# Performance work log

Measured on AMD Instinct MI355X. Metric: run time of the kernel, lower is better.

## Reference

```python
import jax, jax.numpy as jnp
import numpy as np
import math

B, S, HID = 1, 2048, 2048
H, KVH, HD = 16, 4, 128
LEVEL = 256


def _rope_tables(seq_len, dim, dtype=jnp.float32):
    inv_freq = 1.0 / (10000.0 ** (np.arange(0, dim, 2, dtype=np.float32) / dim))
    ang = np.arange(seq_len, dtype=np.float32)[:, None] * inv_freq[None, :]  # [S, HD/2]
    emb = np.concatenate([ang, ang], axis=-1)  # [S, HD]
    return jnp.asarray(np.cos(emb), dtype)[None], jnp.asarray(np.sin(emb), dtype)[None]


def setup_inputs() -> dict:
    key = jax.random.key(0)
    ks = jax.random.split(key, 6)
    hidden_states = jax.random.normal(ks[0], (B, S, HID), jnp.float32)
    w_std = 1.0 / math.sqrt(HID)
    Wq = jax.random.normal(ks[1], (H * HD, HID), jnp.float32) * w_std
    Wk = jax.random.normal(ks[2], (KVH * HD, HID), jnp.float32) * w_std
    Wv = jax.random.normal(ks[3], (KVH * HD, HID), jnp.float32) * w_std
    Wo = jax.random.normal(ks[4], (HID, H * HD), jnp.float32) * w_std
    cos, sin = _rope_tables(S, HD)
    # additive causal mask [1,1,S,S]
    tri = jnp.tril(jnp.ones((S, S), jnp.bool_))
    attention_mask = jnp.where(tri, 0.0, -1e9).astype(jnp.float32)[None, None]
    return {
        "hidden_states": hidden_states,
        "Wq": Wq, "Wk": Wk, "Wv": Wv, "Wo": Wo,
        "s_q": jnp.full((1,), 0.05, jnp.float32),
        "s_k": jnp.full((1,), 0.05, jnp.float32),
        "s_v": jnp.full((1,), 0.05, jnp.float32),
        "s_attn": jnp.full((1,), 0.004, jnp.float32),
        "s_out": jnp.full((1,), 0.02, jnp.float32),
        "cos": cos, "sin": sin,
        "attention_mask": attention_mask,
    }


def _lsq(x, s, level, sym):
    # LSQ fake-quant: learned per-tensor step s, STE round, LSQ grad-scale on s.
    if sym:
        qn, qp = -level // 2, level // 2 - 1
    else:
        qn, qp = 0, level - 1
    g = 1.0 / math.sqrt(x.size * qp)          # LSQ gradient scale (static)
    s = jnp.abs(s)
    s_eff = s * g + jax.lax.stop_gradient(s - s * g)  # fwd = s, bwd grad *= g
    v = jnp.clip(x / s_eff, qn, qp)
    q = v + jax.lax.stop_gradient(jnp.round(v) - v)   # STE round
    return q * s_eff


def _rotate_half(x):
    x1, x2 = jnp.split(x, 2, axis=-1)
    return jnp.concatenate([-x2, x1], axis=-1)


def _attn_fwd(hidden_states, Wq, Wk, Wv, Wo, s_q, s_k, s_v, s_attn, s_out,
              cos, sin, attention_mask):
    b, s_len, _ = hidden_states.shape
    # projections -> [B, heads, S, HD]
    q = (hidden_states @ Wq.T).reshape(b, s_len, H, HD).transpose(0, 2, 1, 3)
    q = _lsq(q, s_q, LEVEL, sym=True)
    k = (hidden_states @ Wk.T).reshape(b, s_len, KVH, HD).transpose(0, 2, 1, 3)
    k = _lsq(k, s_k, LEVEL, sym=True)
    v = (hidden_states @ Wv.T).reshape(b, s_len, KVH, HD).transpose(0, 2, 1, 3)
    v = _lsq(v, s_v, LEVEL, sym=True)
    # RoPE (after quant, matching source order)
    c, si = cos[:, None], sin[:, None]  # [B,1,S,HD]
    q = q * c + _rotate_half(q) * si
    k = k * c + _rotate_half(k) * si
    # GQA repeat
    groups = H // KVH
    k = jnp.repeat(k, groups, axis=1)
    v = jnp.repeat(v, groups, axis=1)
    scores = jnp.einsum("bhqd,bhkd->bhqk", q, k) / math.sqrt(HD)
    scores = scores + attention_mask[:, :, :, :s_len]
    attn = jax.nn.softmax(scores.astype(jnp.float32), axis=-1).astype(q.dtype)
    attn = _lsq(attn, s_attn, LEVEL, sym=False)
    out = jnp.einsum("bhqk,bhkd->bhqd", attn, v)
    out = _lsq(out, s_out, LEVEL, sym=False)
    out = out.transpose(0, 2, 1, 3).reshape(b, s_len, H * HD)
    out = out @ Wo.T
    return out, attn


def reference(hidden_states, Wq, Wk, Wv, Wo, s_q, s_k, s_v, s_attn, s_out,
              cos, sin, attention_mask):
    return _attn_fwd(hidden_states, Wq, Wk, Wv, Wo, s_q, s_k, s_v, s_attn,
                     s_out, cos, sin, attention_mask)
```

## Files before the change

kernel.cpp:

```cpp
#include <hip/hip_runtime.h>
#include <math.h>

#define S_LEN 2048
#define HID_DIM 2048
#define NH 16
#define NKVH 4
#define HD 128
#define QD (NH*HD)
#define KD (NKVH*HD)
#define NQKV 3072

typedef _Float16 half8_t __attribute__((ext_vector_type(8)));
typedef _Float16 half4_t __attribute__((ext_vector_type(4)));
typedef float f32x4 __attribute__((ext_vector_type(4)));

#define BM 128
#define BN 128
#define BK 32
#define KCHUNK 512

typedef const __attribute__((address_space(1))) char gas_char;
typedef __attribute__((address_space(3))) char las_char;
#define GL16(gp, lp) __builtin_amdgcn_global_load_lds((gas_char*)(gp), (las_char*)(lp), 16, 0, 0)

template<int LA, int LB, bool AF32, bool PSM, bool ATOMK>
__global__ __launch_bounds__(256)
void gemm_f16(const void* __restrict__ Ap, const _Float16* __restrict__ Alo,
              int lda, long long strA,
              const _Float16* __restrict__ Bhi, const _Float16* __restrict__ Blo,
              int ldb, long long strB, int divB,
              void* __restrict__ Cp, int ldc, long long strC,
              int K, float scale_c, const float* sc1, const float* sc2,
              const float* preAp,
              int qmode, const float* q1, const float* q2, const float* q3,
              int causal, int triK, float* __restrict__ pml)
{
    int bz = blockIdx.z;
    int m0 = blockIdx.y * BM;
    int n0 = ATOMK ? 0 : blockIdx.x * BN;
    if (causal && n0 > m0 + (BM - 1)) return;
    int Keff = K;
    if (triK && (m0 + BM) < Keff) Keff = m0 + BM;

    int kbeg = 0, kend = Keff;
    if constexpr (ATOMK) {
        kbeg = blockIdx.x * KCHUNK;
        kend = min(Keff, kbeg + KCHUNK);
        if (kbeg >= kend) return;
    }

    const _Float16* Ahi = AF32 ? nullptr : (const _Float16*)Ap + bz * strA;
    const _Float16* AloP = (LA == 2) ? Alo + bz * strA : nullptr;
    const float* Af = AF32 ? (const float*)Ap + bz * strA : nullptr;
    const _Float16* BhiP = Bhi + (long long)(bz / divB) * strB;
    const _Float16* BloP = (LB == 2) ? Blo + (long long)(bz / divB) * strB : nullptr;
    float* Cf = (float*)Cp + bz * strC;
    _Float16* Ch = (_Float16*)Cp + bz * strC;

    float preA = 1.f;
    if (AF32) preA = 1.f / fabsf(preAp[0]);

    __shared__ _Float16 lds[(LA + LB) * 4096];
    _Float16* As0 = lds;
    _Float16* As1 = lds + 4096;
    _Float16* Bs0 = lds + LA * 4096;
    _Float16* Bs1 = lds + (LA + 1) * 4096;

    int t = threadIdx.x;
    int srow = t >> 2;
    int gsw = (srow >> 1) & 3;
    int gc = ((t & 3) ^ gsw) * 8;
    int w = t >> 6, lane = t & 63;
    int wm = (w >> 1) * 64, wn = (w & 1) * 64;
    int lr = lane & 15, lg = lane >> 4;
    int fco = ((lg ^ ((lr >> 1) & 3))) * 8;

    f32x4 acc[4][4];
    #pragma unroll
    for (int i = 0; i < 4; ++i)
        #pragma unroll
        for (int j = 0; j < 4; ++j)
            acc[i][j] = (f32x4){0.f, 0.f, 0.f, 0.f};

    for (int k0 = kbeg; k0 < kend; k0 += BK) {
        f32x4 aF[2][2];
        if constexpr (AF32) {
            #pragma unroll
            for (int rep = 0; rep < 2; ++rep) {
                long long ai = (long long)(m0 + rep * 64 + srow) * lda + k0 + gc;
                aF[rep][0] = *(const f32x4*)&Af[ai];
                aF[rep][1] = *(const f32x4*)&Af[ai + 4];
            }
        }
        __syncthreads();
        #pragma unroll
        for (int rep = 0; rep < 2; ++rep) {
            int row = rep * 64 + srow;
            int lo = rep * 2048 + t * 8;
            if constexpr (!AF32) {
                long long ai = (long long)(m0 + row) * lda + k0 + gc;
                GL16(Ahi + ai, As0 + lo);
                if constexpr (LA == 2) GL16(AloP + ai, As1 + lo);
            }
            long long bi = (long long)(n0 + row) * ldb + k0 + gc;
            GL16(BhiP + bi, Bs0 + lo);
            if constexpr (LB == 2) GL16(BloP + bi, Bs1 + lo);
        }
        if constexpr (AF32) {
            #pragma unroll
            for (int rep = 0; rep < 2; ++rep) {
                half8_t h;
                #pragma unroll
                for (int e = 0; e < 4; ++e) {
                    h[e]     = (_Float16)(aF[rep][0][e] * preA);
                    h[e + 4] = (_Float16)(aF[rep][1][e] * preA);
                }
                *(half8_t*)&As0[rep * 2048 + t * 8] = h;
            }
        }
        __syncthreads();

        half8_t a0[4], b0[4];
        #pragma unroll
        for (int i = 0; i < 4; ++i) a0[i] = *(const half8_t*)&As0[(wm + i*16 + lr) * 32 + fco];
        #pragma unroll
        for (int j = 0; j < 4; ++j) b0[j] = *(const half8_t*)&Bs0[(wn + j*16 + lr) * 32 + fco];
        #pragma unroll
        for (int i = 0; i < 4; ++i)
            #pragma unroll
            for (int j = 0; j < 4; ++j)
                acc[i][j] = __builtin_amdgcn_mfma_f32_16x16x32_f16(a0[i], b0[j], acc[i][j], 0, 0, 0);
        if constexpr (LB == 2) {
            half8_t b1[4];
            #pragma unroll
            for (int j = 0; j < 4; ++j) b1[j] = *(const half8_t*)&Bs1[(wn + j*16 + lr) * 32 + fco];
            #pragma unroll
            for (int i = 0; i < 4; ++i)
                #pragma unroll
                for (int j = 0; j < 4; ++j)
                    acc[i][j] = __builtin_amdgcn_mfma_f32_16x16x32_f16(a0[i], b1[j], acc[i][j], 0, 0, 0);
        }
        if constexpr (LA == 2) {
            half8_t a1[4];
            #pragma unroll
            for (int i = 0; i < 4; ++i) a1[i] = *(const half8_t*)&As1[(wm + i*16 + lr) * 32 + fco];
            #pragma unroll
            for (int i = 0; i < 4; ++i)
                #pragma unroll
                for (int j = 0; j < 4; ++j)
                    acc[i][j] = __builtin_amdgcn_mfma_f32_16x16x32_f16(a1[i], b0[j], acc[i][j], 0, 0, 0);
        }
    }

    if constexpr (ATOMK) {
        #pragma unroll
        for (int i = 0; i < 4; ++i)
            #pragma unroll
            for (int j = 0; j < 4; ++j)
                #pragma unroll
                for (int r = 0; r < 4; ++r) {
                    long long row = m0 + wm + i * 16 + lg * 4 + r;
                    long long col = n0 + wn + j * 16 + lr;
                    atomicAdd(&Cf[row * (long long)ldc + col], acc[i][j][r]);
                }
        return;
    }

    float se = scale_c;
    if (sc1) se *= fabsf(sc1[0]);
    if (sc2) se *= fabsf(sc2[0]);
    float sv = 1.f;
    if (qmode == 3) {
        const float* sp = (n0 < 2048) ? q1 : ((n0 < 2560) ? q2 : q3);
        sv = fabsf(sp[0]);
        qmode = 1;
    } else if (qmode) {
        sv = fabsf(q1[0]);
    }

    #pragma unroll
    for (int i = 0; i < 4; ++i)
        #pragma unroll
        for (int j = 0; j < 4; ++j)
            #pragma unroll
            for (int r = 0; r < 4; ++r) {
                long long row = m0 + wm + i * 16 + lg * 4 + r;
                long long col = n0 + wn + j * 16 + lr;
                float v = acc[i][j][r] * se;
                if (qmode == 0) {
                    Cf[row * (long long)ldc + col] = v;
                } else if (qmode == 1) {
                    float u = rintf(fminf(fmaxf(v / sv, -128.f), 127.f));
                    Ch[row * (long long)ldc + col] = (_Float16)u;
                } else {
                    float u = rintf(fminf(fmaxf(v / sv, 0.f), 255.f));
                    Ch[row * (long long)ldc + col] = (_Float16)u;
                }
            }

    if constexpr (PSM) {
        int cb64 = (n0 + wn) >> 6;
        #pragma unroll
        for (int i = 0; i < 4; ++i)
            #pragma unroll
            for (int r = 0; r < 4; ++r) {
                int row = m0 + wm + i * 16 + lg * 4 + r;
                float vv[4];
                float mloc = -INFINITY;
                #pragma unroll
                for (int j = 0; j < 4; ++j) {
                    int col = n0 + wn + j * 16 + lr;
                    float v = acc[i][j][r] * se;
                    vv[j] = (col <= row) ? v : -INFINITY;
                    mloc = fmaxf(mloc, vv[j]);
                }
                #pragma unroll
                for (int o = 1; o < 16; o <<= 1) mloc = fmaxf(mloc, __shfl_xor(mloc, o));
                float sloc = 0.f;
                #pragma unroll
                for (int j = 0; j < 4; ++j) sloc += expf(vv[j] - mloc);
                #pragma unroll
                for (int o = 1; o < 16; o <<= 1) sloc += __shfl_xor(sloc, o);
                if (lr == 0) {
                    long long idx = (((long long)bz * S_LEN + row) * 32 + cb64) * 2;
                    pml[idx] = mloc;
                    pml[idx + 1] = sloc;
                }
            }
    }
}

__global__ __launch_bounds__(256)
void reduce_ml(const float* __restrict__ pml, float* __restrict__ fml)
{
    int id = blockIdx.x * 256 + threadIdx.x;
    int r = id & (S_LEN - 1);
    int nb = (r >> 6) + 1;
    float m = -INFINITY, l = 0.f;
    const float* p = pml + (long long)id * 64;
    for (int cb = 0; cb < nb; ++cb) {
        float mp = p[cb * 2], lp = p[cb * 2 + 1];
        float mn = fmaxf(m, mp);
        l = l * expf(m - mn) + lp * expf(mp - mn);
        m = mn;
    }
    fml[id * 2] = m;
    fml[id * 2 + 1] = l;
}

__global__ __launch_bounds__(256)
void finalize_quant(float* __restrict__ attn, const float* __restrict__ fml,
                    const float* __restrict__ s_at_p)
{
    int row = blockIdx.x;
    int q = row & (S_LEN - 1);
    float* p = attn + (long long)row * S_LEN;
    float m = fml[row * 2];
    float l = fml[row * 2 + 1];
    float sa = fabsf(s_at_p[0]);
    int t = threadIdx.x;
    #pragma unroll
    for (int c = t * 4; c < S_LEN; c += 1024) {
        f32x4 v = *(const f32x4*)&p[c];
        f32x4 o;
        #pragma unroll
        for (int e = 0; e < 4; ++e) {
            float u = 0.f;
            if (c + e <= q) {
                float pr = expf(v[e] - m) / l;
                u = rintf(fminf(fmaxf(pr / sa, 0.f), 255.f));
            }
            o[e] = u * sa;
        }
        *(f32x4*)&p[c] = o;
    }
}

__global__ __launch_bounds__(256)
void quant_ao(const float* __restrict__ acc, _Float16* __restrict__ ao,
              const float* sa_p, const float* sv_p, const float* so_p)
{
    int i = blockIdx.x * 256 + threadIdx.x;
    float seo = fabsf(sa_p[0]) * fabsf(sv_p[0]) / fabsf(so_p[0]);
    f32x4 v = ((const f32x4*)acc)[i];
    half4_t o;
    #pragma unroll
    for (int e = 0; e < 4; ++e)
        o[e] = (_Float16)rintf(fminf(fmaxf(v[e] * seo, 0.f), 255.f));
    ((half4_t*)ao)[i] = o;
}

__global__ void split_f16(const float* __restrict__ in, _Float16* __restrict__ hi,
                          _Float16* __restrict__ lo, int n4)
{
    int i = blockIdx.x * 256 + threadIdx.x;
    if (i >= n4) return;
    f32x4 v = ((const f32x4*)in)[i];
    half4_t h, l;
    #pragma unroll
    for (int e = 0; e < 4; ++e) {
        h[e] = (_Float16)v[e];
        l[e] = (_Float16)(v[e] - (float)h[e]);
    }
    ((half4_t*)hi)[i] = h;
    ((half4_t*)lo)[i] = l;
}

__global__ void rope_f16(const _Float16* __restrict__ codes, int ldc_, int colOff,
                         const float* __restrict__ cosT,
                         const float* __restrict__ sinT,
                         _Float16* __restrict__ ohi, _Float16* __restrict__ olo, int nh)
{
    long long idx = (long long)blockIdx.x * 256 + threadIdx.x;
    int d = idx & (HD - 1);
    long long tt = idx >> 7;
    int h = (int)(tt % nh);
    int s = (int)(tt / nh);
    long long base = (long long)s * ldc_ + colOff + h * HD;
    float x = (float)codes[base + d];
    float other = (d < 64) ? -(float)codes[base + d + 64] : (float)codes[base + d - 64];
    float o = x * cosT[s * HD + d] + other * sinT[s * HD + d];
    _Float16 hf = (_Float16)o;
    long long oi = ((long long)h * S_LEN + s) * HD + d;
    ohi[oi] = hf;
    olo[oi] = (_Float16)(o - (float)hf);
}

__global__ __launch_bounds__(256)
void transpose_vf16(const _Float16* __restrict__ in, _Float16* __restrict__ outp)
{
    __shared__ _Float16 tile[64][72];
    int s0 = blockIdx.x * 64, d0 = blockIdx.y * 64, h = blockIdx.z;
    int t = threadIdx.x;
    int rr = t >> 4, cc = (t & 15) * 4;
    #pragma unroll
    for (int r = 0; r < 4; ++r) {
        half4_t v = *(const half4_t*)&in[(long long)(s0 + rr + 16*r) * NQKV + 2560 + h * HD + d0 + cc];
        *(half4_t*)&tile[rr + 16*r][cc] = v;
    }
    __syncthreads();
    #pragma unroll
    for (int r = 0; r < 4; ++r) {
        int dr = rr + 16 * r;
        half4_t o = { tile[cc+0][dr], tile[cc+1][dr], tile[cc+2][dr], tile[cc+3][dr] };
        *(half4_t*)&outp[((long long)h * HD + d0 + dr) * S_LEN + s0 + cc] = o;
    }
}

extern "C" void kernel_launch(void* const* d_in, const int* in_sizes, int n_in,
                              void* d_out, int out_size, void* d_ws, size_t ws_size,
                              hipStream_t stream)
{
    const float* hs    = (const float*)d_in[0];
    const float* Wq    = (const float*)d_in[1];
    const float* Wk    = (const float*)d_in[2];
    const float* Wv    = (const float*)d_in[3];
    const float* Wo    = (const float*)d_in[4];
    const float* s_q   = (const float*)d_in[5];
    const float* s_k   = (const float*)d_in[6];
    const float* s_v   = (const float*)d_in[7];
    const float* s_at  = (const float*)d_in[8];
    const float* s_out = (const float*)d_in[9];
    const float* cosT  = (const float*)d_in[10];
    const float* sinT  = (const float*)d_in[11];

    float* out  = (float*)d_out;
    float* attn = out + (long long)S_LEN * HID_DIM;

    const long long M1 = 1LL * 1024 * 1024;
    const long long M4 = 4LL * M1;
    const long long M6 = 6LL * M1;

    _Float16* wsh   = (_Float16*)d_ws;
    _Float16* qr_hi = wsh;
    _Float16* qr_lo = qr_hi + M4;
    _Float16* kr_hi = qr_lo + M4;
    _Float16* kr_lo = kr_hi + M1;
    _Float16* vT    = kr_lo + M1;
    _Float16* ao    = vT + M1;
    _Float16* Wo_hi = ao + M4;
    _Float16* Wo_lo = Wo_hi + M4;
    float*    ao_acc = (float*)(Wo_lo + M4);

    _Float16* sc      = (_Float16*)attn;
    _Float16* hs_hi   = sc;
    _Float16* hs_lo   = hs_hi + M4;
    _Float16* Whi     = hs_lo + M4;
    _Float16* Wlo     = Whi + M6;
    _Float16* qkvcode = Wlo + M6;

    float* pml = out;
    float* fml = out + 2LL * 1024 * 1024;

    dim3 blk(256);
    const float iscale = 0.08838834764831845f;

    split_f16<<<4096, blk, 0, stream>>>(hs, hs_hi, hs_lo, 1024*1024);
    split_f16<<<4096, blk, 0, stream>>>(Wq, Whi, Wlo, 1024*1024);
    split_f16<<<1024, blk, 0, stream>>>(Wk, Whi + 2048LL*2048, Wlo + 2048LL*2048, 256*1024);
    split_f16<<<1024, blk, 0, stream>>>(Wv, Whi + 2560LL*2048, Wlo + 2560LL*2048, 256*1024);
    split_f16<<<4096, blk, 0, stream>>>(Wo, Wo_hi, Wo_lo, 1024*1024);

    gemm_f16<2,2,false,false,false><<<dim3(NQKV/BN, S_LEN/BM, 1), blk, 0, stream>>>(
        hs_hi, hs_lo, HID_DIM, 0, Whi, Wlo, HID_DIM, 0, 1,
        qkvcode, NQKV, 0, HID_DIM, 1.f, nullptr, nullptr, nullptr,
        3, s_q, s_k, s_v, 0, 0, nullptr);

    rope_f16<<<(NH*S_LEN*HD)/256, blk, 0, stream>>>(qkvcode, NQKV, 0, cosT, sinT, qr_hi, qr_lo, NH);
    rope_f16<<<(NKVH*S_LEN*HD)/256, blk, 0, stream>>>(qkvcode, NQKV, 2048, cosT, sinT, kr_hi, kr_lo, NKVH);
    transpose_vf16<<<dim3(S_LEN/64, HD/64, NKVH), blk, 0, stream>>>(qkvcode, vT);

    gemm_f16<2,2,false,true,false><<<dim3(S_LEN/BN, S_LEN/BM, NH), blk, 0, stream>>>(
        qr_hi, qr_lo, HD, (long long)S_LEN*HD,
        kr_hi, kr_lo, HD, (long long)S_LEN*HD, NH/NKVH,
        attn, S_LEN, (long long)S_LEN*S_LEN,
        HD, iscale, s_q, s_k, nullptr, 0, nullptr, nullptr, nullptr, 1, 0, pml);

    reduce_ml<<<(NH*S_LEN)/256, blk, 0, stream>>>(pml, fml);

    finalize_quant<<<NH*S_LEN, blk, 0, stream>>>(attn, fml, s_at);

    hipMemsetAsync(ao_acc, 0, (size_t)S_LEN * QD * sizeof(float), stream);
    gemm_f16<1,1,true,false,true><<<dim3(S_LEN/KCHUNK, S_LEN/BM, NH), blk, 0, stream>>>(
        attn, nullptr, S_LEN, (long long)S_LEN*S_LEN,
        vT, nullptr, S_LEN, (long long)HD*S_LEN, NH/NKVH,
        ao_acc, QD, HD,
        S_LEN, 1.f, nullptr, nullptr, s_at, 0, nullptr, nullptr, nullptr, 0, 1, nullptr);
    quant_ao<<<(S_LEN*QD)/1024, blk, 0, stream>>>(ao_acc, ao, s_at, s_v, s_out);

    gemm_f16<1,2,false,false,false><<<dim3(HID_DIM/BN, S_LEN/BM, 1), blk, 0, stream>>>(
        ao, nullptr, QD, 0, Wo_hi, Wo_lo, QD, 0, 1,
        out, HID_DIM, 0, QD, 1.f, s_out, nullptr, nullptr,
        0, nullptr, nullptr, nullptr, 0, 0, nullptr);
}
```

Baseline: 557.7 us.

## Persistent per-row-tile scores kernel with online softmax stats; drop split-K atomics for PV

Replaces the grid-wide QK^T GEMM with partial max/sum outputs and the separate reduce kernel by a persistent kernel per 128-row tile and head. It keeps Q resident in LDS and low-part Q in registers, streams K tiles with double buffering, and accumulates running softmax max/sum in registers. The causal-masked upper triangle is zeroed in finalize_quant, which now reads only up to the diagonal. The PV GEMM drops the split-K atomics, memset and quant_ao pass and quantizes in its epilogue. The risks are less parallelism in the scores kernel (256 blocks with uneven causal work) and longer serial K loops in PV.

```diff
diff --git a/kernel.cpp b/kernel.cpp
--- a/kernel.cpp
+++ b/kernel.cpp
@@ -17,13 +17,12 @@
 #define BM 128
 #define BN 128
 #define BK 32
-#define KCHUNK 512
 
 typedef const __attribute__((address_space(1))) char gas_char;
 typedef __attribute__((address_space(3))) char las_char;
 #define GL16(gp, lp) __builtin_amdgcn_global_load_lds((gas_char*)(gp), (las_char*)(lp), 16, 0, 0)
 
-template<int LA, int LB, bool AF32, bool PSM, bool ATOMK>
+template<int LA, int LB, bool AF32>
 __global__ __launch_bounds__(256)
 void gemm_f16(const void* __restrict__ Ap, const _Float16* __restrict__ Alo,
               int lda, long long strA,
@@ -33,21 +32,13 @@
               int K, float scale_c, const float* sc1, const float* sc2,
               const float* preAp,
               int qmode, const float* q1, const float* q2, const float* q3,
-              int causal, int triK, float* __restrict__ pml)
+              int causal, int triK)
 {
     int bz = blockIdx.z;
-    int m0 = blockIdx.y * BM;
-    int n0 = ATOMK ? 0 : blockIdx.x * BN;
+    int m0 = blockIdx.y * BM, n0 = blockIdx.x * BN;
     if (causal && n0 > m0 + (BM - 1)) return;
     int Keff = K;
     if (triK && (m0 + BM) < Keff) Keff = m0 + BM;
-
-    int kbeg = 0, kend = Keff;
-    if constexpr (ATOMK) {
-        kbeg = blockIdx.x * KCHUNK;
-        kend = min(Keff, kbeg + KCHUNK);
-        if (kbeg >= kend) return;
-    }
 
     const _Float16* Ahi = AF32 ? nullptr : (const _Float16*)Ap + bz * strA;
     const _Float16* AloP = (LA == 2) ? Alo + bz * strA : nullptr;
@@ -82,7 +73,7 @@
         for (int j = 0; j < 4; ++j)
             acc[i][j] = (f32x4){0.f, 0.f, 0.f, 0.f};
 
-    for (int k0 = kbeg; k0 < kend; k0 += BK) {
+    for (int k0 = 0; k0 < Keff; k0 += BK) {
         f32x4 aF[2][2];
         if constexpr (AF32) {
             #pragma unroll
@@ -150,20 +141,6 @@
                 for (int j = 0; j < 4; ++j)
                     acc[i][j] = __builtin_amdgcn_mfma_f32_16x16x32_f16(a1[i], b0[j], acc[i][j], 0, 0, 0);
         }
-    }
-
-    if constexpr (ATOMK) {
-        #pragma unroll
-        for (int i = 0; i < 4; ++i)
-            #pragma unroll
-            for (int j = 0; j < 4; ++j)
-                #pragma unroll
-                for (int r = 0; r < 4; ++r) {
-                    long long row = m0 + wm + i * 16 + lg * 4 + r;
-                    long long col = n0 + wn + j * 16 + lr;
-                    atomicAdd(&Cf[row * (long long)ldc + col], acc[i][j][r]);
-                }
-        return;
     }
 
     float se = scale_c;
@@ -197,55 +174,182 @@
                     Ch[row * (long long)ldc + col] = (_Float16)u;
                 }
             }
-
-    if constexpr (PSM) {
-        int cb64 = (n0 + wn) >> 6;
+}
+
+__global__ __launch_bounds__(256)
+void scores_persist(const _Float16* __restrict__ qhi, const _Float16* __restrict__ qlo,
+                    const _Float16* __restrict__ khi, const _Float16* __restrict__ klo,
+                    float* __restrict__ attn, float* __restrict__ fml,
+                    const float* sq_p, const float* sk_p)
+{
+    __shared__ _Float16 lds[32768];
+    _Float16* Qh = lds;
+    _Float16* Bb = lds + 16384;
+
+    int mt = blockIdx.x, h = blockIdx.y;
+    int m0 = mt * 128;
+    const _Float16* Qhg = qhi + (long long)h * S_LEN * HD;
+    const _Float16* Qlg = qlo + (long long)h * S_LEN * HD;
+    const _Float16* Kh  = khi + (long long)(h >> 2) * S_LEN * HD;
+    const _Float16* Kl  = klo + (long long)(h >> 2) * S_LEN * HD;
+    float* S = attn + (long long)h * S_LEN * S_LEN;
+
+    float se = fabsf(sq_p[0]) * fabsf(sk_p[0]) * 0.08838834764831845f;
+
+    int t = threadIdx.x;
+    int w = t >> 6, lane = t & 63;
+    int wm = (w >> 1) * 64, wn = (w & 1) * 64;
+    int lr = lane & 15, lg = lane >> 4;
+    int srow = t >> 2;
+    int gsw = (srow >> 1) & 3;
+    int gcc = ((t & 3) ^ gsw) * 8;
+    int fco = (lg ^ ((lr >> 1) & 3)) * 8;
+
+    #pragma unroll
+    for (int v = 0; v < 8; ++v) {
+        int s = v * 256 + t;
+        int r = s >> 4, cp = s & 15;
+        int cl = cp ^ (r & 15);
+        GL16(Qhg + (long long)(m0 + r) * HD + cl * 8, Qh + s * 8);
+    }
+
+    half8_t alo[4][4];
+    #pragma unroll
+    for (int i = 0; i < 4; ++i)
+        #pragma unroll
+        for (int ks = 0; ks < 4; ++ks)
+            alo[i][ks] = *(const half8_t*)&Qlg[(long long)(m0 + wm + i*16 + lr) * HD + ks*32 + lg*8];
+
+    auto stageB = [&](int nt, int ks, int b) {
+        #pragma unroll
+        for (int rep = 0; rep < 2; ++rep) {
+            long long bi = (long long)(nt * 128 + rep * 64 + srow) * HD + ks * 32 + gcc;
+            int lo = rep * 2048 + t * 8;
+            GL16(Kh + bi, Bb + (b * 2 + 0) * 4096 + lo);
+            GL16(Kl + bi, Bb + (b * 2 + 1) * 4096 + lo);
+        }
+    };
+
+    stageB(0, 0, 0);
+    asm volatile("s_waitcnt vmcnt(0)" ::: "memory");
+    __builtin_amdgcn_s_barrier();
+    __builtin_amdgcn_sched_barrier(0);
+
+    f32x4 acc[4][4];
+    #pragma unroll
+    for (int i = 0; i < 4; ++i)
+        #pragma unroll
+        for (int j = 0; j < 4; ++j)
+            acc[i][j] = (f32x4){0.f, 0.f, 0.f, 0.f};
+    float mrun[16], lrun[16];
+    #pragma unroll
+    for (int ri = 0; ri < 16; ++ri) { mrun[ri] = -INFINITY; lrun[ri] = 0.f; }
+
+    int nsteps = (mt + 1) * 4;
+    for (int it = 0; it < nsteps; ++it) {
+        int nt = it >> 2, ks = it & 3, buf = it & 1;
+        if (it + 1 < nsteps) {
+            stageB((it + 1) >> 2, (it + 1) & 3, (it + 1) & 1);
+            asm volatile("s_waitcnt vmcnt(4)" ::: "memory");
+        } else {
+            asm volatile("s_waitcnt vmcnt(0)" ::: "memory");
+        }
+        __builtin_amdgcn_s_barrier();
+        __builtin_amdgcn_sched_barrier(0);
+
+        const _Float16* B0 = Bb + (buf * 2 + 0) * 4096;
+        const _Float16* B1 = Bb + (buf * 2 + 1) * 4096;
+        half8_t a0[4], b0[4], b1[4];
         #pragma unroll
         for (int i = 0; i < 4; ++i)
+            a0[i] = *(const half8_t*)&Qh[(wm + i*16 + lr) * 128 + ((ks*4 + lg) ^ lr) * 8];
+        #pragma unroll
+        for (int j = 0; j < 4; ++j) {
+            b0[j] = *(const half8_t*)&B0[(wn + j*16 + lr) * 32 + fco];
+            b1[j] = *(const half8_t*)&B1[(wn + j*16 + lr) * 32 + fco];
+        }
+        #pragma unroll
+        for (int i = 0; i < 4; ++i)
+            #pragma unroll
+            for (int j = 0; j < 4; ++j)
+                acc[i][j] = __builtin_amdgcn_mfma_f32_16x16x32_f16(a0[i], b0[j], acc[i][j], 0, 0, 0);
+        #pragma unroll
+        for (int i = 0; i < 4; ++i)
+            #pragma unroll
+            for (int j = 0; j < 4; ++j)
+                acc[i][j] = __builtin_amdgcn_mfma_f32_16x16x32_f16(a0[i], b1[j], acc[i][j], 0, 0, 0);
+        #pragma unroll
+        for (int i = 0; i < 4; ++i)
+            #pragma unroll
+            for (int j = 0; j < 4; ++j)
+                acc[i][j] = __builtin_amdgcn_mfma_f32_16x16x32_f16(alo[i][ks], b0[j], acc[i][j], 0, 0, 0);
+
+        if (ks == 3) {
+            int n0 = nt * 128;
+            #pragma unroll
+            for (int i = 0; i < 4; ++i)
+                #pragma unroll
+                for (int r = 0; r < 4; ++r) {
+                    int row = m0 + wm + i * 16 + lg * 4 + r;
+                    float vv[4];
+                    float mloc = -INFINITY;
+                    #pragma unroll
+                    for (int j = 0; j < 4; ++j) {
+                        int col = n0 + wn + j * 16 + lr;
+                        float v = acc[i][j][r] * se;
+                        S[(long long)row * S_LEN + col] = v;
+                        vv[j] = (col <= row) ? v : -INFINITY;
+                        mloc = fmaxf(mloc, vv[j]);
+                    }
+                    #pragma unroll
+                    for (int o = 1; o < 16; o <<= 1) mloc = fmaxf(mloc, __shfl_xor(mloc, o));
+                    if (mloc > -INFINITY) {
+                        float sloc = 0.f;
+                        #pragma unroll
+                        for (int j = 0; j < 4; ++j)
+                            sloc += (vv[j] > -INFINITY) ? expf(vv[j] - mloc) : 0.f;
+                        #pragma unroll
+                        for (int o = 1; o < 16; o <<= 1) sloc += __shfl_xor(sloc, o);
+                        int ri = i * 4 + r;
+                        float mn = fmaxf(mrun[ri], mloc);
+                        lrun[ri] = lrun[ri] * expf(mrun[ri] - mn) + sloc * expf(mloc - mn);
+                        mrun[ri] = mn;
+                    }
+                }
+            #pragma unroll
+            for (int i = 0; i < 4; ++i)
+                #pragma unroll
+                for (int j = 0; j < 4; ++j)
+                    acc[i][j] = (f32x4){0.f, 0.f, 0.f, 0.f};
+        }
+        __builtin_amdgcn_s_barrier();
+        __builtin_amdgcn_sched_barrier(0);
+    }
+
+    __syncthreads();
+    float* sm = (float*)Bb;
+    float* sl = sm + 256;
+    if (lr == 0) {
+        #pragma unroll
+        for (int i = 0; i < 4; ++i)
             #pragma unroll
             for (int r = 0; r < 4; ++r) {
-                int row = m0 + wm + i * 16 + lg * 4 + r;
-                float vv[4];
-                float mloc = -INFINITY;
-                #pragma unroll
-                for (int j = 0; j < 4; ++j) {
-                    int col = n0 + wn + j * 16 + lr;
-                    float v = acc[i][j][r] * se;
-                    vv[j] = (col <= row) ? v : -INFINITY;
-                    mloc = fmaxf(mloc, vv[j]);
-                }
-                #pragma unroll
-                for (int o = 1; o < 16; o <<= 1) mloc = fmaxf(mloc, __shfl_xor(mloc, o));
-                float sloc = 0.f;
-                #pragma unroll
-                for (int j = 0; j < 4; ++j) sloc += expf(vv[j] - mloc);
-                #pragma unroll
-                for (int o = 1; o < 16; o <<= 1) sloc += __shfl_xor(sloc, o);
-                if (lr == 0) {
-                    long long idx = (((long long)bz * S_LEN + row) * 32 + cb64) * 2;
-                    pml[idx] = mloc;
-                    pml[idx + 1] = sloc;
-                }
+                int rl = wm + i * 16 + lg * 4 + r;
+                sm[rl * 2 + (wn >> 6)] = mrun[i * 4 + r];
+                sl[rl * 2 + (wn >> 6)] = lrun[i * 4 + r];
             }
     }
-}
-
-__global__ __launch_bounds__(256)
-void reduce_ml(const float* __restrict__ pml, float* __restrict__ fml)
-{
-    int id = blockIdx.x * 256 + threadIdx.x;
-    int r = id & (S_LEN - 1);
-    int nb = (r >> 6) + 1;
-    float m = -INFINITY, l = 0.f;
-    const float* p = pml + (long long)id * 64;
-    for (int cb = 0; cb < nb; ++cb) {
-        float mp = p[cb * 2], lp = p[cb * 2 + 1];
-        float mn = fmaxf(m, mp);
-        l = l * expf(m - mn) + lp * expf(mp - mn);
-        m = mn;
-    }
-    fml[id * 2] = m;
-    fml[id * 2 + 1] = l;
+    __syncthreads();
+    if (t < 128) {
+        float m1 = sm[t * 2], l1 = sl[t * 2];
+        float m2 = sm[t * 2 + 1], l2 = sl[t * 2 + 1];
+        float m, l;
+        if (m2 == -INFINITY) { m = m1; l = l1; }
+        else { m = fmaxf(m1, m2); l = l1 * expf(m1 - m) + l2 * expf(m2 - m); }
+        long long id = (long long)h * S_LEN + m0 + t;
+        fml[id * 2] = m;
+        fml[id * 2 + 1] = l;
+    }
 }
 
 __global__ __launch_bounds__(256)
@@ -259,8 +363,8 @@
     float l = fml[row * 2 + 1];
     float sa = fabsf(s_at_p[0]);
     int t = threadIdx.x;
-    #pragma unroll
-    for (int c = t * 4; c < S_LEN; c += 1024) {
+    int n4 = (q + 4) & ~3;
+    for (int c = t * 4; c < n4; c += 1024) {
         f32x4 v = *(const f32x4*)&p[c];
         f32x4 o;
         #pragma unroll
@@ -274,20 +378,9 @@
         }
         *(f32x4*)&p[c] = o;
     }
-}
-
-__global__ __launch_bounds__(256)
-void quant_ao(const float* __restrict__ acc, _Float16* __restrict__ ao,
-              const float* sa_p, const float* sv_p, const float* so_p)
-{
-    int i = blockIdx.x * 256 + threadIdx.x;
-    float seo = fabsf(sa_p[0]) * fabsf(sv_p[0]) / fabsf(so_p[0]);
-    f32x4 v = ((const f32x4*)acc)[i];
-    half4_t o;
-    #pragma unroll
-    for (int e = 0; e < 4; ++e)
-        o[e] = (_Float16)rintf(fminf(fmaxf(v[e] * seo, 0.f), 255.f));
-    ((half4_t*)ao)[i] = o;
+    f32x4 z = (f32x4){0.f, 0.f, 0.f, 0.f};
+    for (int c = n4 + t * 4; c < S_LEN; c += 1024)
+        *(f32x4*)&p[c] = z;
 }
 
 __global__ void split_f16(const float* __restrict__ in, _Float16* __restrict__ hi,
@@ -380,7 +473,7 @@
     _Float16* ao    = vT + M1;
     _Float16* Wo_hi = ao + M4;
     _Float16* Wo_lo = Wo_hi + M4;
-    float*    ao_acc = (float*)(Wo_lo + M4);
+    float*    fml   = (float*)(Wo_lo + M4);
 
     _Float16* sc      = (_Float16*)attn;
     _Float16* hs_hi   = sc;
@@ -389,11 +482,7 @@
     _Float16* Wlo     = Whi + M6;
     _Float16* qkvcode = Wlo + M6;
 
-    float* pml = out;
-    float* fml = out + 2LL * 1024 * 1024;
-
     dim3 blk(256);
-    const float iscale = 0.08838834764831845f;
 
     split_f16<<<4096, blk, 0, stream>>>(hs, hs_hi, hs_lo, 1024*1024);
     split_f16<<<4096, blk, 0, stream>>>(Wq, Whi, Wlo, 1024*1024);
@@ -401,35 +490,28 @@
     split_f16<<<1024, blk, 0, stream>>>(Wv, Whi + 2560LL*2048, Wlo + 2560LL*2048, 256*1024);
     split_f16<<<4096, blk, 0, stream>>>(Wo, Wo_hi, Wo_lo, 1024*1024);
 
-    gemm_f16<2,2,false,false,false><<<dim3(NQKV/BN, S_LEN/BM, 1), blk, 0, stream>>>(
+    gemm_f16<2,2,false><<<dim3(NQKV/BN, S_LEN/BM, 1), blk, 0, stream>>>(
         hs_hi, hs_lo, HID_DIM, 0, Whi, Wlo, HID_DIM, 0, 1,
         qkvcode, NQKV, 0, HID_DIM, 1.f, nullptr, nullptr, nullptr,
-        3, s_q, s_k, s_v, 0, 0, nullptr);
+        3, s_q, s_k, s_v, 0, 0);
 
     rope_f16<<<(NH*S_LEN*HD)/256, blk, 0, stream>>>(qkvcode, NQKV, 0, cosT, sinT, qr_hi, qr_lo, NH);
     rope_f16<<<(NKVH*S_LEN*HD)/256, blk, 0, stream>>>(qkvcode, NQKV, 2048, cosT, sinT, kr_hi, kr_lo, NKVH);
     transpose_vf16<<<dim3(S_LEN/64, HD/64, NKVH), blk, 0, stream>>>(qkvcode, vT);
 
-    gemm_f16<2,2,false,true,false><<<dim3(S_LEN/BN, S_LEN/BM, NH), blk, 0, stream>>>(
-        qr_hi, qr_lo, HD, (long long)S_LEN*HD,
-        kr_hi, kr_lo, HD, (long long)S_LEN*HD, NH/NKVH,
-        attn, S_LEN, (long long)S_LEN*S_LEN,
-        HD, iscale, s_q, s_k, nullptr, 0, nullptr, nullptr, nullptr, 1, 0, pml);
-
-    reduce_ml<<<(NH*S_LEN)/256, blk, 0, stream>>>(pml, fml);
+    scores_persist<<<dim3(S_LEN/BM, NH), blk, 0, stream>>>(
+        qr_hi, qr_lo, kr_hi, kr_lo, attn, fml, s_q, s_k);
 
     finalize_quant<<<NH*S_LEN, blk, 0, stream>>>(attn, fml, s_at);
 
-    hipMemsetAsync(ao_acc, 0, (size_t)S_LEN * QD * sizeof(float), stream);
-    gemm_f16<1,1,true,false,true><<<dim3(S_LEN/KCHUNK, S_LEN/BM, NH), blk, 0, stream>>>(
+    gemm_f16<1,1,true><<<dim3(1, S_LEN/BM, NH), blk, 0, stream>>>(
         attn, nullptr, S_LEN, (long long)S_LEN*S_LEN,
         vT, nullptr, S_LEN, (long long)HD*S_LEN, NH/NKVH,
-        ao_acc, QD, HD,
-        S_LEN, 1.f, nullptr, nullptr, s_at, 0, nullptr, nullptr, nullptr, 0, 1, nullptr);
-    quant_ao<<<(S_LEN*QD)/1024, blk, 0, stream>>>(ao_acc, ao, s_at, s_v, s_out);
-
-    gemm_f16<1,2,false,false,false><<<dim3(HID_DIM/BN, S_LEN/BM, 1), blk, 0, stream>>>(
+        ao, QD, HD,
+        S_LEN, 1.f, s_at, s_v, s_at, 2, s_out, nullptr, nullptr, 0, 1);
+
+    gemm_f16<1,2,false><<<dim3(HID_DIM/BN, S_LEN/BM, 1), blk, 0, stream>>>(
         ao, nullptr, QD, 0, Wo_hi, Wo_lo, QD, 0, 1,
         out, HID_DIM, 0, QD, 1.f, s_out, nullptr, nullptr,
-        0, nullptr, nullptr, nullptr, 0, 0, nullptr);
-}
+        0, nullptr, nullptr, nullptr, 0, 0);
+}
```

After: 630.5 us. 13.1% more time.

## Drop split-K atomics for PV GEMM and skip masked softmax work

Applied to the files above, without the earlier changes.

The attention-times-V GEMM no longer splits K into chunks with atomic accumulation into an fp32 buffer. Each block now runs the full causal K range and quantizes directly in the epilogue (qmode 2), which removes the memset, the atomics and the separate quant_ao pass. finalize_quant now computes exp and quantize only up to the causal diagonal and writes zeros past it without reading. The trade-off is fewer blocks (16x16) with long, unbalanced K loops in the PV GEMM, which lowers parallelism.

```diff
diff --git a/kernel.cpp b/kernel.cpp
--- a/kernel.cpp
+++ b/kernel.cpp
@@ -17,13 +17,12 @@
 #define BM 128
 #define BN 128
 #define BK 32
-#define KCHUNK 512
 
 typedef const __attribute__((address_space(1))) char gas_char;
 typedef __attribute__((address_space(3))) char las_char;
 #define GL16(gp, lp) __builtin_amdgcn_global_load_lds((gas_char*)(gp), (las_char*)(lp), 16, 0, 0)
 
-template<int LA, int LB, bool AF32, bool PSM, bool ATOMK>
+template<int LA, int LB, bool AF32, bool PSM>
 __global__ __launch_bounds__(256)
 void gemm_f16(const void* __restrict__ Ap, const _Float16* __restrict__ Alo,
               int lda, long long strA,
@@ -36,18 +35,10 @@
               int causal, int triK, float* __restrict__ pml)
 {
     int bz = blockIdx.z;
-    int m0 = blockIdx.y * BM;
-    int n0 = ATOMK ? 0 : blockIdx.x * BN;
+    int m0 = blockIdx.y * BM, n0 = blockIdx.x * BN;
     if (causal && n0 > m0 + (BM - 1)) return;
     int Keff = K;
     if (triK && (m0 + BM) < Keff) Keff = m0 + BM;
-
-    int kbeg = 0, kend = Keff;
-    if constexpr (ATOMK) {
-        kbeg = blockIdx.x * KCHUNK;
-        kend = min(Keff, kbeg + KCHUNK);
-        if (kbeg >= kend) return;
-    }
 
     const _Float16* Ahi = AF32 ? nullptr : (const _Float16*)Ap + bz * strA;
     const _Float16* AloP = (LA == 2) ? Alo + bz * strA : nullptr;
@@ -82,7 +73,7 @@
         for (int j = 0; j < 4; ++j)
             acc[i][j] = (f32x4){0.f, 0.f, 0.f, 0.f};
 
-    for (int k0 = kbeg; k0 < kend; k0 += BK) {
+    for (int k0 = 0; k0 < Keff; k0 += BK) {
         f32x4 aF[2][2];
         if constexpr (AF32) {
             #pragma unroll
@@ -150,20 +141,6 @@
                 for (int j = 0; j < 4; ++j)
                     acc[i][j] = __builtin_amdgcn_mfma_f32_16x16x32_f16(a1[i], b0[j], acc[i][j], 0, 0, 0);
         }
-    }
-
-    if constexpr (ATOMK) {
-        #pragma unroll
-        for (int i = 0; i < 4; ++i)
-            #pragma unroll
-            for (int j = 0; j < 4; ++j)
-                #pragma unroll
-                for (int r = 0; r < 4; ++r) {
-                    long long row = m0 + wm + i * 16 + lg * 4 + r;
-                    long long col = n0 + wn + j * 16 + lr;
-                    atomicAdd(&Cf[row * (long long)ldc + col], acc[i][j][r]);
-                }
-        return;
     }
 
     float se = scale_c;
@@ -259,8 +236,8 @@
     float l = fml[row * 2 + 1];
     float sa = fabsf(s_at_p[0]);
     int t = threadIdx.x;
-    #pragma unroll
-    for (int c = t * 4; c < S_LEN; c += 1024) {
+    int n4 = (q + 4) & ~3;
+    for (int c = t * 4; c < n4; c += 1024) {
         f32x4 v = *(const f32x4*)&p[c];
         f32x4 o;
         #pragma unroll
@@ -274,20 +251,9 @@
         }
         *(f32x4*)&p[c] = o;
     }
-}
-
-__global__ __launch_bounds__(256)
-void quant_ao(const float* __restrict__ acc, _Float16* __restrict__ ao,
-              const float* sa_p, const float* sv_p, const float* so_p)
-{
-    int i = blockIdx.x * 256 + threadIdx.x;
-    float seo = fabsf(sa_p[0]) * fabsf(sv_p[0]) / fabsf(so_p[0]);
-    f32x4 v = ((const f32x4*)acc)[i];
-    half4_t o;
-    #pragma unroll
-    for (int e = 0; e < 4; ++e)
-        o[e] = (_Float16)rintf(fminf(fmaxf(v[e] * seo, 0.f), 255.f));
-    ((half4_t*)ao)[i] = o;
+    f32x4 z = (f32x4){0.f, 0.f, 0.f, 0.f};
+    for (int c = n4 + t * 4; c < S_LEN; c += 1024)
+        *(f32x4*)&p[c] = z;
 }
 
 __global__ void split_f16(const float* __restrict__ in, _Float16* __restrict__ hi,
@@ -380,7 +346,6 @@
     _Float16* ao    = vT + M1;
     _Float16* Wo_hi = ao + M4;
     _Float16* Wo_lo = Wo_hi + M4;
-    float*    ao_acc = (float*)(Wo_lo + M4);
 
     _Float16* sc      = (_Float16*)attn;
     _Float16* hs_hi   = sc;
@@ -401,7 +366,7 @@
     split_f16<<<1024, blk, 0, stream>>>(Wv, Whi + 2560LL*2048, Wlo + 2560LL*2048, 256*1024);
     split_f16<<<4096, blk, 0, stream>>>(Wo, Wo_hi, Wo_lo, 1024*1024);
 
-    gemm_f16<2,2,false,false,false><<<dim3(NQKV/BN, S_LEN/BM, 1), blk, 0, stream>>>(
+    gemm_f16<2,2,false,false><<<dim3(NQKV/BN, S_LEN/BM, 1), blk, 0, stream>>>(
         hs_hi, hs_lo, HID_DIM, 0, Whi, Wlo, HID_DIM, 0, 1,
         qkvcode, NQKV, 0, HID_DIM, 1.f, nullptr, nullptr, nullptr,
         3, s_q, s_k, s_v, 0, 0, nullptr);
@@ -410,7 +375,7 @@
     rope_f16<<<(NKVH*S_LEN*HD)/256, blk, 0, stream>>>(qkvcode, NQKV, 2048, cosT, sinT, kr_hi, kr_lo, NKVH);
     transpose_vf16<<<dim3(S_LEN/64, HD/64, NKVH), blk, 0, stream>>>(qkvcode, vT);
 
-    gemm_f16<2,2,false,true,false><<<dim3(S_LEN/BN, S_LEN/BM, NH), blk, 0, stream>>>(
+    gemm_f16<2,2,false,true><<<dim3(S_LEN/BN, S_LEN/BM, NH), blk, 0, stream>>>(
         qr_hi, qr_lo, HD, (long long)S_LEN*HD,
         kr_hi, kr_lo, HD, (long long)S_LEN*HD, NH/NKVH,
         attn, S_LEN, (long long)S_LEN*S_LEN,
@@ -420,15 +385,13 @@
 
     finalize_quant<<<NH*S_LEN, blk, 0, stream>>>(attn, fml, s_at);
 
-    hipMemsetAsync(ao_acc, 0, (size_t)S_LEN * QD * sizeof(float), stream);
-    gemm_f16<1,1,true,false,true><<<dim3(S_LEN/KCHUNK, S_LEN/BM, NH), blk, 0, stream>>>(
+    gemm_f16<1,1,true,false><<<dim3(1, S_LEN/BM, NH), blk, 0, stream>>>(
         attn, nullptr, S_LEN, (long long)S_LEN*S_LEN,
         vT, nullptr, S_LEN, (long long)HD*S_LEN, NH/NKVH,
-        ao_acc, QD, HD,
-        S_LEN, 1.f, nullptr, nullptr, s_at, 0, nullptr, nullptr, nullptr, 0, 1, nullptr);
-    quant_ao<<<(S_LEN*QD)/1024, blk, 0, stream>>>(ao_acc, ao, s_at, s_v, s_out);
-
-    gemm_f16<1,2,false,false,false><<<dim3(HID_DIM/BN, S_LEN/BM, 1), blk, 0, stream>>>(
+        ao, QD, HD,
+        S_LEN, 1.f, s_at, s_v, s_at, 2, s_out, nullptr, nullptr, 0, 1, nullptr);
+
+    gemm_f16<1,2,false,false><<<dim3(HID_DIM/BN, S_LEN/BM, 1), blk, 0, stream>>>(
         ao, nullptr, QD, 0, Wo_hi, Wo_lo, QD, 0, 1,
         out, HID_DIM, 0, QD, 1.f, s_out, nullptr, nullptr,
         0, nullptr, nullptr, nullptr, 0, 0, nullptr);
```

Result: no change. 551.4 us (-1.1%).
